# Optimization experiments

Measured on AMD Instinct MI355X. Metric: run time of the kernel, lower is better.

## Reference

```python
import jax, jax.numpy as jnp
import numpy as np
from functools import partial

TOP_K = 2
LN_EPS = 1e-5


def setup_inputs() -> dict:
    key = jax.random.key(0)
    ks = jax.random.split(key, 4)
    B, T, H, F, E = 2, 2048, 1024, 4096, 8
    hidden_states = jax.random.normal(ks[0], (B, T, H), dtype=jnp.float32)
    # Router weights: original inits to zeros; use small random so routing is non-degenerate.
    router_w = jax.random.normal(ks[1], (E, H), dtype=jnp.float32) * 0.02
    router_b = jnp.zeros((E,), dtype=jnp.float32)
    W1 = jax.random.normal(ks[2], (E, H, F), dtype=jnp.float32) * (1.0 / np.sqrt(H))
    b1 = jnp.zeros((E, F), dtype=jnp.float32)
    W2 = jax.random.normal(ks[3], (E, F, H), dtype=jnp.float32) * (1.0 / np.sqrt(F))
    b2 = jnp.zeros((E, H), dtype=jnp.float32)
    ln_gamma = jnp.ones((H,), dtype=jnp.float32)
    ln_beta = jnp.zeros((H,), dtype=jnp.float32)
    return {"hidden_states": hidden_states, "router_w": router_w, "router_b": router_b,
            "W1": W1, "b1": b1, "W2": W2, "b2": b2,
            "ln_gamma": ln_gamma, "ln_beta": ln_beta}


def _layer_norm(x, gamma, beta):
    mu = jnp.mean(x, axis=-1, keepdims=True)
    var = jnp.var(x, axis=-1, keepdims=True)
    return (x - mu) * jax.lax.rsqrt(var + LN_EPS) * gamma + beta


def _moe_forward(hidden_states, router_w, router_b, W1, b1, W2, b2, ln_gamma, ln_beta):
    B, T, H = hidden_states.shape
    E = router_w.shape[0]
    N = B * T
    x = hidden_states.reshape(N, H)
    # Router (jitter=0.0, eval mode): logits [N, E]
    logits = x @ router_w.T + router_b
    topk_vals, topk_idx = jax.lax.top_k(logits, TOP_K)        # [N, K]
    topk_w = jax.nn.softmax(topk_vals, axis=-1)               # [N, K]
    # Scatter top-k weights into a dense combine matrix [N, E] (zeros elsewhere).
    probs = jnp.zeros((N, E), dtype=x.dtype).at[jnp.arange(N)[:, None], topk_idx].set(topk_w)
    # Per-expert FFN via scan over the (small, fixed) expert axis; each step is one
    # big GEMM over all tokens weighted by that expert's combine prob (0 for
    # tokens not routed to it) — same math as gather/MLP/scatter with no capacity drop.
    def body(acc, params_e):
        Wa, ba, Wb, bb, pe = params_e          # pe: [N]
        h = jax.nn.gelu(x @ Wa + ba, approximate=False)   # [N, F]
        y = h @ Wb + bb                                    # [N, H]
        return acc + y * pe[:, None], None
    out, _ = jax.lax.scan(body, jnp.zeros_like(x), (W1, b1, W2, b2, probs.T))
    out = out.reshape(B, T, H)
    return _layer_norm(out + hidden_states, ln_gamma, ln_beta)


def reference(hidden_states, router_w, router_b, W1, b1, W2, b2, ln_gamma, ln_beta):
    return _moe_forward(hidden_states, router_w, router_b, W1, b1, W2, b2, ln_gamma, ln_beta)
```

## Files before the change

### kernel.cpp

```cpp
#include <hip/hip_runtime.h>
#include <hip/hip_bf16.h>


typedef unsigned short u16;
typedef unsigned int u32;
typedef __attribute__((ext_vector_type(4))) float f32x4;
typedef __attribute__((ext_vector_type(8))) short s16x8;
typedef __attribute__((ext_vector_type(8))) unsigned short u16x8;

#define GLD16(gp, lp) __builtin_amdgcn_global_load_lds( \
    (const __attribute__((address_space(1))) void*)(gp), \
    (__attribute__((address_space(3))) void*)(lp), 16, 0, 0)

__device__ __forceinline__ u16 f2bf(float f) {
    union { float f; u32 u; } v; v.f = f;
    u32 u = v.u;
    return (u16)((u + 0x7fffu + ((u >> 16) & 1u)) >> 16);
}
__device__ __forceinline__ float bf2f(u16 h) {
    union { u32 u; float f; } v; v.u = ((u32)h) << 16; return v.f;
}

__device__ __forceinline__ float gelu_f(float v) {
    const float u = v * (0.7978845608f + 0.0356774081f * v * v);
    const float t = __expf(-2.0f * u);
    return v * __builtin_amdgcn_rcpf(1.0f + t);
}

__global__ void k_init(int* cc) { if (threadIdx.x < 16) cc[threadIdx.x] = 0; }

__global__ __launch_bounds__(256) void k_router(
    const float* __restrict__ x, const float* __restrict__ rw, const float* __restrict__ rb,
    u16* __restrict__ xb, int* __restrict__ eidx, float* __restrict__ wgt, int* __restrict__ counts)
{
    const int wav = threadIdx.x >> 6, lane = threadIdx.x & 63;
    const int t = blockIdx.x * 4 + wav;
    const float* xt = x + (size_t)t * 1024;
    float acc[8] = {0.f,0.f,0.f,0.f,0.f,0.f,0.f,0.f};
    #pragma unroll
    for (int c = 0; c < 4; c++) {
        const int base = c * 256 + lane * 4;
        const float4 xv = *(const float4*)(xt + base);
        ushort4 pk;
        pk.x = f2bf(xv.x); pk.y = f2bf(xv.y); pk.z = f2bf(xv.z); pk.w = f2bf(xv.w);
        *(ushort4*)(xb + (size_t)t * 1024 + base) = pk;
        #pragma unroll
        for (int e = 0; e < 8; e++) {
            const float4 wv = *(const float4*)(rw + e * 1024 + base);
            acc[e] += xv.x * wv.x + xv.y * wv.y + xv.z * wv.z + xv.w * wv.w;
        }
    }
    #pragma unroll
    for (int e = 0; e < 8; e++) {
        #pragma unroll
        for (int s = 32; s; s >>= 1) acc[e] += __shfl_xor(acc[e], s);
    }
    if (lane == 0) {
        float v0 = -3e38f, v1 = -3e38f; int i0 = 0, i1 = 0;
        #pragma unroll
        for (int e = 0; e < 8; e++) {
            const float l = acc[e] + rb[e];
            if (l > v0) { v1 = v0; i1 = i0; v0 = l; i0 = e; }
            else if (l > v1) { v1 = l; i1 = e; }
        }
        const float w0 = 1.0f / (1.0f + expf(v1 - v0));
        eidx[2 * t] = i0; eidx[2 * t + 1] = i1;
        wgt[2 * t] = w0; wgt[2 * t + 1] = 1.0f - w0;
        atomicAdd(&counts[i0], 1); atomicAdd(&counts[i1], 1);
    }
}

__global__ void k_offsets(const int* __restrict__ counts, int* __restrict__ offsets) {
    if (threadIdx.x == 0) {
        int s = 0;
        for (int e = 0; e < 8; e++) { offsets[e] = s; s += counts[e]; }
        offsets[8] = s;
    }
}

__global__ __launch_bounds__(256) void k_place(
    const int* __restrict__ eidx, const int* __restrict__ offsets, int* __restrict__ cursors,
    int* __restrict__ rows, int* __restrict__ pos_of)
{
    const int a = blockIdx.x * 256 + threadIdx.x;
    const int e = eidx[a];
    const int pos = offsets[e] + atomicAdd(&cursors[e], 1);
    rows[pos] = a >> 1;
    pos_of[a] = pos;
}

__global__ __launch_bounds__(256) void k_transp(
    const float* __restrict__ src, u16* __restrict__ dst, int R, int C)
{
    const int e = blockIdx.z;
    const float* s = src + (size_t)e * R * C;
    u16* d = dst + (size_t)e * R * C;
    const int c = blockIdx.x * 64 + (threadIdx.x >> 2);
    const int r0 = blockIdx.y * 32 + (threadIdx.x & 3) * 8;
    u16x8 v;
    #pragma unroll
    for (int k = 0; k < 8; k++)
        v[k] = f2bf(s[(size_t)(r0 + k) * C + c]);
    *(u16x8*)(d + (size_t)c * R + r0) = v;
}

#define STAGE_T(b, k0) { \
    char* ad = (char*)At + (b) * 8192 + wav * 1024; \
    char* bd = (char*)Bt + (b) * 8192 + wav * 1024; \
    GLD16(a_src0 + (k0), ad); \
    GLD16(a_src1 + (k0), ad + 4096); \
    GLD16(b_src0 + (k0), bd); \
    GLD16(b_src1 + (k0), bd + 4096); }

#define COMPUTE_T(b) { \
    const u16* Abp = Ab + (b) * 4096; \
    const u16* Bbp = Bb + (b) * 4096; \
    s16x8 af[4], bfr[4]; \
    _Pragma("unroll") \
    for (int i = 0; i < 4; i++) { \
        af[i]  = *(const s16x8*)(Abp + i * 512); \
        bfr[i] = *(const s16x8*)(Bbp + i * 512); \
    } \
    __builtin_amdgcn_s_setprio(1); \
    _Pragma("unroll") \
    for (int mi = 0; mi < 4; mi++) \
        _Pragma("unroll") \
        for (int ni = 0; ni < 4; ni++) \
            acc[mi][ni] = __builtin_amdgcn_mfma_f32_16x16x32_bf16(af[mi], bfr[ni], acc[mi][ni], 0, 0, 0); \
    __builtin_amdgcn_s_setprio(0); }

#define VMCNT4 asm volatile("s_waitcnt vmcnt(4)" ::: "memory")
#define VMCNT0 asm volatile("s_waitcnt vmcnt(0)" ::: "memory")
#define BAR __builtin_amdgcn_s_barrier()

__global__ __launch_bounds__(256, 4) void k_gemm1(
    const u16* __restrict__ xb, const u16* __restrict__ W1t, const float* __restrict__ b1,
    u16* __restrict__ hbuf, const int* __restrict__ rows, const int* __restrict__ offsets)
{
    const int fid = blockIdx.x;
    const int swz = (fid & 7) * 1024 + (fid >> 3);
    const int y = swz & 31, xx = (swz >> 5) & 31, e = swz >> 10;

    const int off = offsets[e], cnt = offsets[e + 1] - off;
    const int row0 = y * 128;
    if (row0 >= cnt) return;
    const int n0 = xx * 128;
    const int tid = threadIdx.x;
    const int lane = tid & 63, wav = tid >> 6, lane15 = lane & 15;

    __shared__ u16 At[2][128][32];
    __shared__ u16 Bt[2][128][32];

    const int ar0 = tid >> 2;
    const int cl8 = (((tid & 3) ^ ((tid >> 3) & 3))) * 8;
    const int t0 = rows[off + min(row0 + ar0, cnt - 1)];
    const int t1 = rows[off + min(row0 + ar0 + 64, cnt - 1)];
    const u16* a_src0 = xb + (size_t)t0 * 1024 + cl8;
    const u16* a_src1 = xb + (size_t)t1 * 1024 + cl8;
    const u16* b_src0 = W1t + ((size_t)e * 4096 + n0 + ar0) * 1024 + cl8;
    const u16* b_src1 = b_src0 + (size_t)64 * 1024;

    f32x4 acc[4][4] = {};
    const int wr = wav >> 1, wc = wav & 1;
    const int koff = ((lane >> 4) ^ ((lane >> 1) & 3)) * 8;
    const u16* Ab = &At[0][wr * 64 + lane15][koff];
    const u16* Bb = &Bt[0][wc * 64 + lane15][koff];

    STAGE_T(0, 0);
    int b = 0;
    for (int k0 = 32; k0 < 1024; k0 += 32) {
        STAGE_T(b ^ 1, k0);
        VMCNT4;
        BAR;
        COMPUTE_T(b);
        BAR;
        b ^= 1;
    }
    VMCNT0;
    BAR;
    COMPUTE_T(b);

    const int rb4 = (lane >> 4) * 4;
    const int colbase = n0 + wc * 64 + lane15;
    float bias[4];
    #pragma unroll
    for (int ni = 0; ni < 4; ni++) bias[ni] = b1[e * 4096 + colbase + ni * 16];
    #pragma unroll
    for (int mi = 0; mi < 4; mi++) {
        #pragma unroll
        for (int j = 0; j < 4; j++) {
            const int lrow = wr * 64 + mi * 16 + rb4 + j;
            if (row0 + lrow < cnt) {
                const size_t gr = (size_t)(off + row0 + lrow);
                #pragma unroll
                for (int ni = 0; ni < 4; ni++) {
                    const float v = acc[mi][ni][j] + bias[ni];
                    hbuf[gr * 4096 + colbase + ni * 16] = f2bf(gelu_f(v));
                }
            }
        }
    }
}

__global__ __launch_bounds__(256, 4) void k_gemm2(
    const u16* __restrict__ hbuf, const u16* __restrict__ W2t, const float* __restrict__ b2,
    u16* __restrict__ y0b, u16* __restrict__ y1b, const int* __restrict__ offsets)
{
    const int fid = blockIdx.x;
    const int swz = (fid & 7) * 512 + (fid >> 3);
    const int y = swz & 31, xx = (swz >> 5) & 7, z = swz >> 8;
    const int e = z >> 1, kh = z & 1;

    const int off = offsets[e], cnt = offsets[e + 1] - off;
    const int row0 = y * 128;
    if (row0 >= cnt) return;
    const int n0 = xx * 128;
    const int tid = threadIdx.x;
    const int lane = tid & 63, wav = tid >> 6, lane15 = lane & 15;
    const int kbase = kh * 2048;

    __shared__ u16 At[2][128][32];
    __shared__ u16 Bt[2][128][32];

    const int ar0 = tid >> 2;
    const int cl8 = (((tid & 3) ^ ((tid >> 3) & 3))) * 8;
    const u16* a_src0 = hbuf + (size_t)(off + min(row0 + ar0, cnt - 1)) * 4096 + kbase + cl8;
    const u16* a_src1 = hbuf + (size_t)(off + min(row0 + ar0 + 64, cnt - 1)) * 4096 + kbase + cl8;
    const u16* b_src0 = W2t + ((size_t)e * 1024 + n0 + ar0) * 4096 + kbase + cl8;
    const u16* b_src1 = b_src0 + (size_t)64 * 4096;

    f32x4 acc[4][4] = {};
    const int wr = wav >> 1, wc = wav & 1;
    const int koff = ((lane >> 4) ^ ((lane >> 1) & 3)) * 8;
    const u16* Ab = &At[0][wr * 64 + lane15][koff];
    const u16* Bb = &Bt[0][wc * 64 + lane15][koff];

    STAGE_T(0, 0);
    int b = 0;
    for (int k0 = 32; k0 < 2048; k0 += 32) {
        STAGE_T(b ^ 1, k0);
        VMCNT4;
        BAR;
        COMPUTE_T(b);
        BAR;
        b ^= 1;
    }
    VMCNT0;
    BAR;
    COMPUTE_T(b);

    u16* yy = kh ? y1b : y0b;
    const int rb4 = (lane >> 4) * 4;
    const int colbase = n0 + wc * 64 + lane15;
    float bias[4];
    #pragma unroll
    for (int ni = 0; ni < 4; ni++) bias[ni] = kh ? 0.f : b2[e * 1024 + colbase + ni * 16];
    #pragma unroll
    for (int mi = 0; mi < 4; mi++) {
        #pragma unroll
        for (int j = 0; j < 4; j++) {
            const int lrow = wr * 64 + mi * 16 + rb4 + j;
            if (row0 + lrow < cnt) {
                const size_t gr = (size_t)(off + row0 + lrow);
                #pragma unroll
                for (int ni = 0; ni < 4; ni++)
                    yy[gr * 1024 + colbase + ni * 16] = f2bf(acc[mi][ni][j] + bias[ni]);
            }
        }
    }
}

__global__ __launch_bounds__(256) void k_combine(
    const float* __restrict__ x, const u16* __restrict__ y0b, const u16* __restrict__ y1b,
    const int* __restrict__ pos_of, const float* __restrict__ wgt,
    const float* __restrict__ gamma, const float* __restrict__ beta,
    float* __restrict__ out)
{
    const int t = blockIdx.x;
    const int tid = threadIdx.x;
    const int p0 = pos_of[2 * t], p1 = pos_of[2 * t + 1];
    const float w0 = wgt[2 * t], w1 = wgt[2 * t + 1];
    const int j4 = tid * 4;
    const float4 xv = *(const float4*)(x + (size_t)t * 1024 + j4);
    const ushort4 ua0 = *(const ushort4*)(y0b + (size_t)p0 * 1024 + j4);
    const ushort4 ub0 = *(const ushort4*)(y1b + (size_t)p0 * 1024 + j4);
    const ushort4 ua1 = *(const ushort4*)(y0b + (size_t)p1 * 1024 + j4);
    const ushort4 ub1 = *(const ushort4*)(y1b + (size_t)p1 * 1024 + j4);
    float a0 = xv.x + w0 * (bf2f(ua0.x) + bf2f(ub0.x)) + w1 * (bf2f(ua1.x) + bf2f(ub1.x));
    float a1 = xv.y + w0 * (bf2f(ua0.y) + bf2f(ub0.y)) + w1 * (bf2f(ua1.y) + bf2f(ub1.y));
    float a2 = xv.z + w0 * (bf2f(ua0.z) + bf2f(ub0.z)) + w1 * (bf2f(ua1.z) + bf2f(ub1.z));
    float a3 = xv.w + w0 * (bf2f(ua0.w) + bf2f(ub0.w)) + w1 * (bf2f(ua1.w) + bf2f(ub1.w));
    float s = a0 + a1 + a2 + a3;
    float q = a0 * a0 + a1 * a1 + a2 * a2 + a3 * a3;
    #pragma unroll
    for (int o = 32; o; o >>= 1) { s += __shfl_xor(s, o); q += __shfl_xor(q, o); }
    __shared__ float ls[4], lq[4];
    const int wav = tid >> 6, lane = tid & 63;
    if (lane == 0) { ls[wav] = s; lq[wav] = q; }
    __syncthreads();
    s = ls[0] + ls[1] + ls[2] + ls[3];
    q = lq[0] + lq[1] + lq[2] + lq[3];
    const float mu = s * (1.0f / 1024.0f);
    const float var = q * (1.0f / 1024.0f) - mu * mu;
    const float rs = rsqrtf(var + 1e-5f);
    const float4 g = *(const float4*)(gamma + j4);
    const float4 b = *(const float4*)(beta + j4);
    float4 o4;
    o4.x = (a0 - mu) * rs * g.x + b.x;
    o4.y = (a1 - mu) * rs * g.y + b.y;
    o4.z = (a2 - mu) * rs * g.z + b.z;
    o4.w = (a3 - mu) * rs * g.w + b.w;
    *(float4*)(out + (size_t)t * 1024 + j4) = o4;
}

extern "C" void kernel_launch(void* const* d_in, const int* in_sizes, int n_in,
                              void* d_out, int out_size, void* d_ws, size_t ws_size,
                              hipStream_t stream) {
    const float* x     = (const float*)d_in[0];
    const float* rw    = (const float*)d_in[1];
    const float* rb    = (const float*)d_in[2];
    const float* W1    = (const float*)d_in[3];
    const float* b1    = (const float*)d_in[4];
    const float* W2    = (const float*)d_in[5];
    const float* b2    = (const float*)d_in[6];
    const float* gamma = (const float*)d_in[7];
    const float* beta  = (const float*)d_in[8];
    float* out = (float*)d_out;

    char* p = (char*)d_ws;
    auto alloc = [&](size_t bytes) { char* r = p; p += (bytes + 255) & ~(size_t)255; return r; };
    int*   counts  = (int*)alloc(16 * sizeof(int));
    int*   cursors = counts + 8;
    int*   offsets = (int*)alloc(9 * sizeof(int));
    int*   eidx    = (int*)alloc(8192 * sizeof(int));
    float* wgt     = (float*)alloc(8192 * sizeof(float));
    int*   pos_of  = (int*)alloc(8192 * sizeof(int));
    int*   rows    = (int*)alloc(8192 * sizeof(int));
    u16*   xb      = (u16*)alloc((size_t)4096 * 1024 * 2);
    u16*   W1t     = (u16*)alloc((size_t)8 * 4096 * 1024 * 2);
    u16*   W2t     = (u16*)alloc((size_t)8 * 1024 * 4096 * 2);
    u16*   hbuf    = (u16*)alloc((size_t)8192 * 4096 * 2);
    u16* y0b = W1t;
    u16* y1b = W1t + (size_t)8192 * 1024;

    hipLaunchKernelGGL(k_init, dim3(1), dim3(64), 0, stream, counts);
    hipLaunchKernelGGL(k_router, dim3(1024), dim3(256), 0, stream, x, rw, rb, xb, eidx, wgt, counts);
    hipLaunchKernelGGL(k_offsets, dim3(1), dim3(64), 0, stream, counts, offsets);
    hipLaunchKernelGGL(k_place, dim3(32), dim3(256), 0, stream, eidx, offsets, cursors, rows, pos_of);
    hipLaunchKernelGGL(k_transp, dim3(64, 32, 8), dim3(256), 0, stream, W1, W1t, 1024, 4096);
    hipLaunchKernelGGL(k_transp, dim3(16, 128, 8), dim3(256), 0, stream, W2, W2t, 4096, 1024);
    hipLaunchKernelGGL(k_gemm1, dim3(8192), dim3(256), 0, stream, xb, W1t, b1, hbuf, rows, offsets);
    hipLaunchKernelGGL(k_gemm2, dim3(4096), dim3(256), 0, stream, hbuf, W2t, b2, y0b, y1b, offsets);
    hipLaunchKernelGGL(k_combine, dim3(4096), dim3(256), 0, stream, x, y0b, y1b, pos_of, wgt, gamma, beta, out);
}
```

Baseline: 460.5 us.

## Triple-buffer GEMM k-loop and tile weight transpose through shared memory

Both expert GEMMs move from a double-buffered to a triple-buffered LDS pipeline that prefetches two k-steps ahead, with vmcnt waits adjusted to match, so global loads have more time to land before the MFMAs need them. Launch bounds drop from 4 to 3 blocks per SM because of the larger shared footprint. Separately, the fp32-to-bf16 weight transpose now stages 64x64 tiles in padded shared memory, so both its reads and writes are coalesced and vectorized instead of strided. The cost is lower occupancy in the GEMMs and an extra barrier in the transpose.

```diff
diff --git a/kernel.cpp b/kernel.cpp
--- a/kernel.cpp
+++ b/kernel.cpp
@@ -92,16 +92,37 @@
 __global__ __launch_bounds__(256) void k_transp(
     const float* __restrict__ src, u16* __restrict__ dst, int R, int C)
 {
+    __shared__ float tl[64][66];
     const int e = blockIdx.z;
     const float* s = src + (size_t)e * R * C;
     u16* d = dst + (size_t)e * R * C;
-    const int c = blockIdx.x * 64 + (threadIdx.x >> 2);
-    const int r0 = blockIdx.y * 32 + (threadIdx.x & 3) * 8;
-    u16x8 v;
-    #pragma unroll
-    for (int k = 0; k < 8; k++)
-        v[k] = f2bf(s[(size_t)(r0 + k) * C + c]);
-    *(u16x8*)(d + (size_t)c * R + r0) = v;
+    const int c0 = blockIdx.x * 64, r0 = blockIdx.y * 64;
+    const int tid = threadIdx.x;
+
+    const int rrow = tid >> 4, rc4 = (tid & 15) * 4;
+    #pragma unroll
+    for (int j = 0; j < 4; j++) {
+        const float4 v = *(const float4*)(s + (size_t)(r0 + rrow + j * 16) * C + c0 + rc4);
+        tl[rc4 + 0][rrow + j * 16] = v.x;
+        tl[rc4 + 1][rrow + j * 16] = v.y;
+        tl[rc4 + 2][rrow + j * 16] = v.z;
+        tl[rc4 + 3][rrow + j * 16] = v.w;
+    }
+    __syncthreads();
+
+    const int wcol = tid >> 3, wr8 = (tid & 7) * 8;
+    #pragma unroll
+    for (int j = 0; j < 2; j++) {
+        const int cc = wcol + j * 32;
+        u16x8 o;
+        #pragma unroll
+        for (int k = 0; k < 4; k++) {
+            const float2 f = *(const float2*)(&tl[cc][wr8 + k * 2]);
+            o[k * 2] = f2bf(f.x);
+            o[k * 2 + 1] = f2bf(f.y);
+        }
+        *(u16x8*)(d + (size_t)(c0 + cc) * R + r0 + wr8) = o;
+    }
 }
 
 #define STAGE_T(b, k0) { \
@@ -129,11 +150,28 @@
             acc[mi][ni] = __builtin_amdgcn_mfma_f32_16x16x32_bf16(af[mi], bfr[ni], acc[mi][ni], 0, 0, 0); \
     __builtin_amdgcn_s_setprio(0); }
 
+#define VMCNT8 asm volatile("s_waitcnt vmcnt(8)" ::: "memory")
 #define VMCNT4 asm volatile("s_waitcnt vmcnt(4)" ::: "memory")
 #define VMCNT0 asm volatile("s_waitcnt vmcnt(0)" ::: "memory")
 #define BAR __builtin_amdgcn_s_barrier()
 
-__global__ __launch_bounds__(256, 4) void k_gemm1(
+#define KLOOP(NSTEP) { \
+    STAGE_T(0, 0); \
+    STAGE_T(1, 32); \
+    int cur = 0, nxt = 2; \
+    for (int t = 0; t < (NSTEP); ++t) { \
+        if (t + 2 < (NSTEP)) { \
+            STAGE_T(nxt, (t + 2) * 32); \
+            nxt = (nxt == 2) ? 0 : nxt + 1; \
+            VMCNT8; \
+        } else if (t + 1 < (NSTEP)) { VMCNT4; } else { VMCNT0; } \
+        BAR; \
+        COMPUTE_T(cur); \
+        cur = (cur == 2) ? 0 : cur + 1; \
+        BAR; \
+    } }
+
+__global__ __launch_bounds__(256, 3) void k_gemm1(
     const u16* __restrict__ xb, const u16* __restrict__ W1t, const float* __restrict__ b1,
     u16* __restrict__ hbuf, const int* __restrict__ rows, const int* __restrict__ offsets)
 {
@@ -148,8 +186,8 @@
     const int tid = threadIdx.x;
     const int lane = tid & 63, wav = tid >> 6, lane15 = lane & 15;
 
-    __shared__ u16 At[2][128][32];
-    __shared__ u16 Bt[2][128][32];
+    __shared__ u16 At[3][128][32];
+    __shared__ u16 Bt[3][128][32];
 
     const int ar0 = tid >> 2;
     const int cl8 = (((tid & 3) ^ ((tid >> 3) & 3))) * 8;
@@ -166,19 +204,7 @@
     const u16* Ab = &At[0][wr * 64 + lane15][koff];
     const u16* Bb = &Bt[0][wc * 64 + lane15][koff];
 
-    STAGE_T(0, 0);
-    int b = 0;
-    for (int k0 = 32; k0 < 1024; k0 += 32) {
-        STAGE_T(b ^ 1, k0);
-        VMCNT4;
-        BAR;
-        COMPUTE_T(b);
-        BAR;
-        b ^= 1;
-    }
-    VMCNT0;
-    BAR;
-    COMPUTE_T(b);
+    KLOOP(32);
 
     const int rb4 = (lane >> 4) * 4;
     const int colbase = n0 + wc * 64 + lane15;
@@ -202,7 +228,7 @@
     }
 }
 
-__global__ __launch_bounds__(256, 4) void k_gemm2(
+__global__ __launch_bounds__(256, 3) void k_gemm2(
     const u16* __restrict__ hbuf, const u16* __restrict__ W2t, const float* __restrict__ b2,
     u16* __restrict__ y0b, u16* __restrict__ y1b, const int* __restrict__ offsets)
 {
@@ -219,8 +245,8 @@
     const int lane = tid & 63, wav = tid >> 6, lane15 = lane & 15;
     const int kbase = kh * 2048;
 
-    __shared__ u16 At[2][128][32];
-    __shared__ u16 Bt[2][128][32];
+    __shared__ u16 At[3][128][32];
+    __shared__ u16 Bt[3][128][32];
 
     const int ar0 = tid >> 2;
     const int cl8 = (((tid & 3) ^ ((tid >> 3) & 3))) * 8;
@@ -235,19 +261,7 @@
     const u16* Ab = &At[0][wr * 64 + lane15][koff];
     const u16* Bb = &Bt[0][wc * 64 + lane15][koff];
 
-    STAGE_T(0, 0);
-    int b = 0;
-    for (int k0 = 32; k0 < 2048; k0 += 32) {
-        STAGE_T(b ^ 1, k0);
-        VMCNT4;
-        BAR;
-        COMPUTE_T(b);
-        BAR;
-        b ^= 1;
-    }
-    VMCNT0;
-    BAR;
-    COMPUTE_T(b);
+    KLOOP(64);
 
     u16* yy = kh ? y1b : y0b;
     const int rb4 = (lane >> 4) * 4;
@@ -347,8 +361,8 @@
     hipLaunchKernelGGL(k_router, dim3(1024), dim3(256), 0, stream, x, rw, rb, xb, eidx, wgt, counts);
     hipLaunchKernelGGL(k_offsets, dim3(1), dim3(64), 0, stream, counts, offsets);
     hipLaunchKernelGGL(k_place, dim3(32), dim3(256), 0, stream, eidx, offsets, cursors, rows, pos_of);
-    hipLaunchKernelGGL(k_transp, dim3(64, 32, 8), dim3(256), 0, stream, W1, W1t, 1024, 4096);
-    hipLaunchKernelGGL(k_transp, dim3(16, 128, 8), dim3(256), 0, stream, W2, W2t, 4096, 1024);
+    hipLaunchKernelGGL(k_transp, dim3(64, 16, 8), dim3(256), 0, stream, W1, W1t, 1024, 4096);
+    hipLaunchKernelGGL(k_transp, dim3(16, 64, 8), dim3(256), 0, stream, W2, W2t, 4096, 1024);
     hipLaunchKernelGGL(k_gemm1, dim3(8192), dim3(256), 0, stream, xb, W1t, b1, hbuf, rows, offsets);
     hipLaunchKernelGGL(k_gemm2, dim3(4096), dim3(256), 0, stream, hbuf, W2t, b2, y0b, y1b, offsets);
     hipLaunchKernelGGL(k_combine, dim3(4096), dim3(256), 0, stream, x, y0b, y1b, pos_of, wgt, gamma, beta, out);
```

Result: slower. 475.6 us (+3.3%).
